# Kernel tuning notes

Measured on AMD Instinct MI355X. Metric: run time of the kernel, lower is better.

## Reference

```python
import jax, jax.numpy as jnp
import numpy as np

KERNEL_SIZE = 13
SIGMA_MIN, SIGMA_MAX = 0.4, 10.0
BETA, THRESHOLD = 0.95, 1.0


@jax.custom_vjp
def spike(x):
    # Heaviside forward, snntorch ATan surrogate backward (alpha=2)
    return (x > 0).astype(x.dtype)

def _spike_fwd(x):
    return spike(x), x

def _spike_bwd(x, g):
    return (g / (1.0 + (jnp.pi * x) ** 2),)

spike.defvjp(_spike_fwd, _spike_bwd)


def setup_inputs() -> dict:
    key = jax.random.key(0)
    k1, k2 = jax.random.split(key)
    B, C, T = 32, 224, 2048
    inp = jax.random.normal(k1, (B, 1, C, T), dtype=jnp.float32)
    linear_w = jax.random.normal(k2, (1, C), dtype=jnp.float32) * (1.0 / np.sqrt(C))
    return {"inp": inp, "linear_w": linear_w}


def _forward(inp, linear_w):
    x = inp[:, 0]  # [B, C, T]
    B, C, T = x.shape
    sigma_mean = 0.5 * (SIGMA_MIN + SIGMA_MAX)
    # adaptive sigma per (batch, time): Linear over channel axis, no bias
    w = sigma_mean + jnp.einsum('bct,c->bt', x, linear_w[0]) * (SIGMA_MAX - SIGMA_MIN)
    w = jnp.clip(w, SIGMA_MIN, SIGMA_MAX)  # [B, T]

    half = KERNEL_SIZE // 2
    r = jnp.linspace(-half, half, KERNEL_SIZE)
    r_all = jnp.linspace(-half * 10, half * 10, KERNEL_SIZE * 10)
    sig = w[..., None]  # [B, T, 1]
    kern = jnp.exp(-0.5 * (r / sig) ** 2)                       # [B, T, K]
    norm = jnp.exp(-0.5 * (r_all / sig) ** 2).sum(-1, keepdims=True)
    kern = kern / norm                                          # normalized over fine grid

    # adaptive gaussian smoothing along the CHANNEL axis (per timestep kernel)
    xt = jnp.transpose(x, (0, 2, 1))                            # [B, T, C]
    padded = jnp.pad(xt, ((0, 0), (0, 0), (half, half)))        # zero pad channels
    x_mean = sum(padded[:, :, k:k + C] * kern[:, :, k:k + 1]
                 for k in range(KERNEL_SIZE))                   # [B, T, C]
    x_mean = jnp.transpose(x_mean, (0, 2, 1))                   # [B, C, T]

    I = x - jax.nn.relu(x - x_mean)                             # soft min(x, x_mean)

    # Leaky-integrate-and-fire over time (snntorch Leaky, reset-by-subtract)
    def step(mem, I_t):
        reset = jax.lax.stop_gradient((mem > THRESHOLD).astype(I_t.dtype))
        mem = BETA * mem + I_t - reset * THRESHOLD
        spk = spike(mem - THRESHOLD)
        return mem, spk

    I_seq = jnp.transpose(I, (2, 0, 1))                         # [T, B, C]
    _, spk = jax.lax.scan(step, jnp.zeros((B, C), I.dtype), I_seq)
    spk = jnp.transpose(spk, (1, 2, 0))                         # [B, C, T]
    return spk[:, None]                                         # [B, 1, C, T]


def reference(inp, linear_w):
    return _forward(inp, linear_w)
```

## Files before the change

kernel.cpp:

```cpp
#include <hip/hip_runtime.h>
#include <math.h>

#define BB 32
#define CCH 224
#define TTT 2048
#define BT (BB*TTT)
#define TPB 64
#define NT  (TTT/TPB)
#define CG  28
#define NCG (CCH/CG)
#define IROW 29
#define RD 4

__global__ __launch_bounds__(256) void kw(
    const float* __restrict__ x, const float* __restrict__ lw,
    double* __restrict__ kernG)
{
    __shared__ double sd[16][64];
    __shared__ float  lws[CCH];
    const int b   = blockIdx.y;
    const int t0  = blockIdx.x * 64;
    const int tid = threadIdx.x;

    if (tid < CCH) lws[tid] = lw[tid];
    __syncthreads();

    {
        const int q = tid & 15, g = tid >> 4;
        const float* xb = x + (((size_t)(b * CCH + g * 14)) << 11) + t0 + 4 * q;
        double a0 = 0, a1 = 0, a2 = 0, a3 = 0;
        #pragma unroll
        for (int i = 0; i < 14; ++i) {
            float4 v = *(const float4*)(xb + ((size_t)i << 11));
            double wv = (double)lws[g * 14 + i];
            a0 += (double)v.x * wv;
            a1 += (double)v.y * wv;
            a2 += (double)v.z * wv;
            a3 += (double)v.w * wv;
        }
        sd[g][4 * q + 0] = a0; sd[g][4 * q + 1] = a1;
        sd[g][4 * q + 2] = a2; sd[g][4 * q + 3] = a3;
    }
    __syncthreads();

    if (tid < 64) {
        const int t = tid;
        double s2 = 0.0;
        #pragma unroll
        for (int g = 0; g < 16; ++g) s2 += sd[g][t];

        double w = 5.2 + s2 * 9.6;
        w = fmin(fmax(w, 0.4), 10.0);
        double iw2 = 1.0 / (w * w);

        const double s = 120.0 / 129.0;
        double G  = exp(-0.125 * s * s * iw2);
        double G2 = G * G, G4 = G2 * G2, G8 = G4 * G4;
        double term = G, cmul = G8, norm = G;
        for (int u = 1; u <= 64; ++u) { term *= cmul; cmul *= G8; norm += term; }
        norm *= 2.0;

        double P = exp(-0.5 * iw2), P2 = P * P;
        double a = 1.0, bm = P, inv = 1.0 / norm;
        double* kr = kernG + (size_t)b * TTT + t0 + t;
        kr[0] = inv;
        #pragma unroll
        for (int d = 1; d <= 6; ++d) {
            a *= bm; bm *= P2;
            kr[(size_t)d * BT] = a * inv;
        }
    }
}

#define PF(h,s) ((h)*RD+(s))
#define CF(s)   (8+(s))
#define SF(s)   (12+(s))
#define OW(s)   (16+(s))

__global__ __launch_bounds__(256) void kf(
    const float* __restrict__ x, const double* __restrict__ kernG,
    float* __restrict__ out)
{
    __shared__ double Is[RD][TPB][IROW];
    __shared__ unsigned long long bitsb[RD][CG];
    __shared__ int fl[32];

    const int b    = blockIdx.y;
    const int c0   = blockIdx.x * CG;
    const int tid  = threadIdx.x;
    const int wid  = tid >> 6;
    const int lane = tid & 63;

    if (tid < 32) fl[tid] = 0;
    __syncthreads();

    const float*  xbase = x + (((size_t)(b * CCH)) << 11);
    const double* kbase = kernG + (size_t)b * TTT;
    float* obase = out + (((size_t)(b * CCH + c0)) << 11);

    if (wid == 1 || wid == 2) {
        const int h  = wid - 1;
        const int cb = 14 * h;
        const int crow0 = c0 + cb - 6;
        float  xc[26], xn[26];
        double kc[7],  kn[7];

        #pragma unroll
        for (int i = 0; i < 26; ++i) {
            int cr = crow0 + i;
            xc[i] = (cr >= 0 && cr < CCH) ? xbase[((size_t)cr << 11) + lane] : 0.0f;
        }
        #pragma unroll
        for (int d = 0; d < 7; ++d) kc[d] = kbase[(size_t)d * BT + lane];

        #pragma unroll 1
        for (int k = 0; k < NT; ++k) {
            if (k + 1 < NT) {
                const int gt = (k + 1) * TPB + lane;
                #pragma unroll
                for (int i = 0; i < 26; ++i) {
                    int cr = crow0 + i;
                    xn[i] = (cr >= 0 && cr < CCH) ? xbase[((size_t)cr << 11) + gt] : 0.0f;
                }
                #pragma unroll
                for (int d = 0; d < 7; ++d) kn[d] = kbase[(size_t)d * BT + gt];
            }
            double iv[14];
            #pragma unroll
            for (int c = 0; c < 14; ++c) {
                double acc = 0.0;
                #pragma unroll
                for (int kk = 0; kk < 13; ++kk) {
                    int d = kk < 6 ? 6 - kk : kk - 6;
                    acc = fma((double)xc[c + kk], kc[d], acc);
                }
                double xvv = (double)xc[c + 6];
                double dd  = xvv - acc;
                iv[c] = xvv - (dd > 0.0 ? dd : 0.0);
            }
            const int s = k & (RD - 1);
            while (__hip_atomic_load(&fl[CF(s)], __ATOMIC_ACQUIRE,
                                     __HIP_MEMORY_SCOPE_WORKGROUP) < k + 1 - RD)
                __builtin_amdgcn_s_sleep(1);
            #pragma unroll
            for (int c = 0; c < 14; ++c) Is[s][lane][cb + c] = iv[c];
            if (lane == 0)
                __hip_atomic_store(&fl[PF(h, s)], k + 1, __ATOMIC_RELEASE,
                                   __HIP_MEMORY_SCOPE_WORKGROUP);
            if (k + 1 < NT) {
                #pragma unroll
                for (int i = 0; i < 26; ++i) xc[i] = xn[i];
                #pragma unroll
                for (int d = 0; d < 7; ++d) kc[d] = kn[d];
            }
        }
    } else if (wid == 0) {
        const int c    = lane;
        const int cidx = (c < CG) ? c : 0;
        double mem = 0.0;
        bool   r   = false;

        #pragma unroll 1
        for (int k = 0; k < NT; ++k) {
            const int s = k & (RD - 1);
            while (__hip_atomic_load(&fl[PF(0, s)], __ATOMIC_ACQUIRE,
                                     __HIP_MEMORY_SCOPE_WORKGROUP) < k + 1 ||
                   __hip_atomic_load(&fl[PF(1, s)], __ATOMIC_ACQUIRE,
                                     __HIP_MEMORY_SCOPE_WORKGROUP) < k + 1)
                __builtin_amdgcn_s_sleep(1);

            unsigned long long bits = 0ull;
            {
                double va[8], vam[8], vb[8], vbm[8];
                #pragma unroll
                for (int j = 0; j < 8; ++j) {
                    va[j] = Is[s][j][cidx]; vam[j] = va[j] - 1.0;
                }
                #pragma unroll
                for (int g = 0; g < 64; g += 16) {
                    #pragma unroll
                    for (int j = 0; j < 8; ++j) {
                        vb[j] = Is[s][g + 8 + j][cidx]; vbm[j] = vb[j] - 1.0;
                    }
                    #pragma unroll
                    for (int j = 0; j < 8; ++j) {
                        double m1 = fma(0.95, mem, va[j]);
                        double m2 = fma(0.95, mem, vam[j]);
                        mem = r ? m2 : m1;
                        r = mem > 1.0;
                        bits |= (unsigned long long)(r ? 1 : 0) << (g + j);
                    }
                    if (g + 16 < 64) {
                        #pragma unroll
                        for (int j = 0; j < 8; ++j) {
                            va[j] = Is[s][g + 16 + j][cidx]; vam[j] = va[j] - 1.0;
                        }
                    }
                    #pragma unroll
                    for (int j = 0; j < 8; ++j) {
                        double m1 = fma(0.95, mem, vb[j]);
                        double m2 = fma(0.95, mem, vbm[j]);
                        mem = r ? m2 : m1;
                        r = mem > 1.0;
                        bits |= (unsigned long long)(r ? 1 : 0) << (g + 8 + j);
                    }
                }
            }
            if (lane == 0)
                __hip_atomic_store(&fl[CF(s)], k + 1, __ATOMIC_RELEASE,
                                   __HIP_MEMORY_SCOPE_WORKGROUP);

            while (__hip_atomic_load(&fl[OW(s)], __ATOMIC_ACQUIRE,
                                     __HIP_MEMORY_SCOPE_WORKGROUP) < k + 1 - RD)
                __builtin_amdgcn_s_sleep(1);
            if (c < CG) bitsb[s][c] = bits;
            if (lane == 0)
                __hip_atomic_store(&fl[SF(s)], k + 1, __ATOMIC_RELEASE,
                                   __HIP_MEMORY_SCOPE_WORKGROUP);
        }
    } else {
        const int qq = lane & 15;
        #pragma unroll 1
        for (int k = 0; k < NT; ++k) {
            const int s = k & (RD - 1);
            while (__hip_atomic_load(&fl[SF(s)], __ATOMIC_ACQUIRE,
                                     __HIP_MEMORY_SCOPE_WORKGROUP) < k + 1)
                __builtin_amdgcn_s_sleep(1);
            unsigned long long bb[7];
            #pragma unroll
            for (int i = 0; i < 7; ++i) {
                int cc = (lane >> 4) + 4 * i;
                bb[i] = bitsb[s][cc];
            }
            if (lane == 0)
                __hip_atomic_store(&fl[OW(s)], k + 1, __ATOMIC_RELEASE,
                                   __HIP_MEMORY_SCOPE_WORKGROUP);
            #pragma unroll
            for (int i = 0; i < 7; ++i) {
                int cc = (lane >> 4) + 4 * i;
                unsigned long long bv = bb[i] >> (4 * qq);
                float4 v;
                v.x = (bv & 1ull) ? 1.0f : 0.0f;
                v.y = (bv & 2ull) ? 1.0f : 0.0f;
                v.z = (bv & 4ull) ? 1.0f : 0.0f;
                v.w = (bv & 8ull) ? 1.0f : 0.0f;
                *(float4*)(obase + ((size_t)cc << 11) + k * TPB + 4 * qq) = v;
            }
        }
    }
}

extern "C" void kernel_launch(void* const* d_in, const int* in_sizes, int n_in,
                              void* d_out, int out_size, void* d_ws, size_t ws_size,
                              hipStream_t stream)
{
    const float* x  = (const float*)d_in[0];
    const float* lw = (const float*)d_in[1];
    float* out = (float*)d_out;

    double* kernG = (double*)d_ws;

    kw<<<dim3(TTT / 64, BB), 256, 0, stream>>>(x, lw, kernG);
    kf<<<dim3(NCG, BB), 256, 0, stream>>>(x, kernG, out);
}
```

Baseline: 157.5 us.

## Use volatile LDS spin flags, ping-pong conv buffers, and retile sigma kernel

Replaces the workgroup-scope atomic acquire/release flag polling and s_sleep in the warp-specialized pipeline with volatile LDS spins plus explicit lgkmcnt waits and compiler fences. The goal is lower handoff latency between the conv warps, the LIF scan warp and the store warp. The conv loop is unrolled by two with A/B register buffers, which removes the per-iteration prefetch register copies. The sigma/kernel-weight kernel now covers 256 timesteps per block with all 256 threads computing the normalisation, using fewer blocks and less idle work. Busy spinning without sleep can steal issue slots from co-resident waves, and the hand-written fences carry memory-ordering risk.

```diff
diff --git a/kernel.cpp b/kernel.cpp
--- a/kernel.cpp
+++ b/kernel.cpp
@@ -12,46 +12,51 @@
 #define IROW 29
 #define RD 4
 
+#define PF(h,s) ((h)*RD+(s))
+#define CF(s)   (8+(s))
+#define SF(s)   (12+(s))
+#define OW(s)   (16+(s))
+
+#define LDS_REL() asm volatile("s_waitcnt lgkmcnt(0)" ::: "memory")
+#define CFENCE()  asm volatile("" ::: "memory")
+
 __global__ __launch_bounds__(256) void kw(
     const float* __restrict__ x, const float* __restrict__ lw,
     double* __restrict__ kernG)
 {
-    __shared__ double sd[16][64];
+    __shared__ double sd[4][256];
     __shared__ float  lws[CCH];
-    const int b   = blockIdx.y;
-    const int t0  = blockIdx.x * 64;
-    const int tid = threadIdx.x;
+    const int b    = blockIdx.y;
+    const int t0   = blockIdx.x << 8;
+    const int tid  = threadIdx.x;
+    const int w    = tid >> 6, lane = tid & 63;
 
     if (tid < CCH) lws[tid] = lw[tid];
     __syncthreads();
 
     {
-        const int q = tid & 15, g = tid >> 4;
-        const float* xb = x + (((size_t)(b * CCH + g * 14)) << 11) + t0 + 4 * q;
+        const float* xb = x + (((size_t)(b * CCH + w)) << 11) + t0 + 4 * lane;
         double a0 = 0, a1 = 0, a2 = 0, a3 = 0;
-        #pragma unroll
-        for (int i = 0; i < 14; ++i) {
-            float4 v = *(const float4*)(xb + ((size_t)i << 11));
-            double wv = (double)lws[g * 14 + i];
+        #pragma unroll 8
+        for (int i = 0; i < 56; ++i) {
+            float4 v = *(const float4*)(xb + ((size_t)(4 * i) << 11));
+            double wv = (double)lws[w + 4 * i];
             a0 += (double)v.x * wv;
             a1 += (double)v.y * wv;
             a2 += (double)v.z * wv;
             a3 += (double)v.w * wv;
         }
-        sd[g][4 * q + 0] = a0; sd[g][4 * q + 1] = a1;
-        sd[g][4 * q + 2] = a2; sd[g][4 * q + 3] = a3;
+        sd[w][4 * lane + 0] = a0; sd[w][4 * lane + 1] = a1;
+        sd[w][4 * lane + 2] = a2; sd[w][4 * lane + 3] = a3;
     }
     __syncthreads();
 
-    if (tid < 64) {
-        const int t = tid;
-        double s2 = 0.0;
-        #pragma unroll
-        for (int g = 0; g < 16; ++g) s2 += sd[g][t];
-
-        double w = 5.2 + s2 * 9.6;
-        w = fmin(fmax(w, 0.4), 10.0);
-        double iw2 = 1.0 / (w * w);
+    {
+        double s2 = (sd[0][tid] + sd[1][tid]) + (sd[2][tid] + sd[3][tid]);
+
+        double w2 = 5.2 + s2 * 9.6;
+        w2 = fmin(fmax(w2, 0.4), 10.0);
+        double iw2 = 1.0 / (w2 * w2);
 
         const double s = 120.0 / 129.0;
         double G  = exp(-0.125 * s * s * iw2);
@@ -62,7 +67,7 @@
 
         double P = exp(-0.5 * iw2), P2 = P * P;
         double a = 1.0, bm = P, inv = 1.0 / norm;
-        double* kr = kernG + (size_t)b * TTT + t0 + t;
+        double* kr = kernG + (size_t)b * TTT + t0 + tid;
         kr[0] = inv;
         #pragma unroll
         for (int d = 1; d <= 6; ++d) {
@@ -72,10 +77,41 @@
     }
 }
 
-#define PF(h,s) ((h)*RD+(s))
-#define CF(s)   (8+(s))
-#define SF(s)   (12+(s))
-#define OW(s)   (16+(s))
+#define CONV_BODY(K, XC, KC, XN, KN)                                       \
+    {                                                                      \
+        const int k_ = (K);                                                \
+        if (k_ + 1 < NT) {                                                 \
+            const int gt = (k_ + 1) * TPB + lane;                          \
+            _Pragma("unroll")                                              \
+            for (int i = 0; i < 26; ++i) {                                 \
+                int cr = crow0 + i;                                        \
+                XN[i] = (cr >= 0 && cr < CCH)                              \
+                    ? xbase[((size_t)cr << 11) + gt] : 0.0f;               \
+            }                                                              \
+            _Pragma("unroll")                                              \
+            for (int d = 0; d < 7; ++d)                                    \
+                KN[d] = kbase[(size_t)d * BT + gt];                        \
+        }                                                                  \
+        double iv[14];                                                     \
+        _Pragma("unroll")                                                  \
+        for (int c = 0; c < 14; ++c) {                                     \
+            double acc = 0.0;                                              \
+            _Pragma("unroll")                                              \
+            for (int kk = 0; kk < 13; ++kk) {                              \
+                int d = kk < 6 ? 6 - kk : kk - 6;                          \
+                acc = fma((double)XC[c + kk], KC[d], acc);                 \
+            }                                                              \
+            double xvv = (double)XC[c + 6];                                \
+            double dd  = xvv - acc;                                        \
+            iv[c] = xvv - (dd > 0.0 ? dd : 0.0);                           \
+        }                                                                  \
+        const int s_ = k_ & (RD - 1);                                      \
+        while (vfl[CF(s_)] < k_ + 1 - RD) {}                               \
+        CFENCE();                                                          \
+        _Pragma("unroll")                                                  \
+        for (int c = 0; c < 14; ++c) Is[s_][lane][cb + c] = iv[c];         \
+        if (lane == 0) { LDS_REL(); vfl[PF(h, s_)] = k_ + 1; }             \
+    }
 
 __global__ __launch_bounds__(256) void kf(
     const float* __restrict__ x, const double* __restrict__ kernG,
@@ -84,6 +120,7 @@
     __shared__ double Is[RD][TPB][IROW];
     __shared__ unsigned long long bitsb[RD][CG];
     __shared__ int fl[32];
+    volatile int* vfl = fl;
 
     const int b    = blockIdx.y;
     const int c0   = blockIdx.x * CG;
@@ -102,57 +139,21 @@
         const int h  = wid - 1;
         const int cb = 14 * h;
         const int crow0 = c0 + cb - 6;
-        float  xc[26], xn[26];
-        double kc[7],  kn[7];
+        float  xcA[26], xcB[26];
+        double kcA[7],  kcB[7];
 
         #pragma unroll
         for (int i = 0; i < 26; ++i) {
             int cr = crow0 + i;
-            xc[i] = (cr >= 0 && cr < CCH) ? xbase[((size_t)cr << 11) + lane] : 0.0f;
+            xcA[i] = (cr >= 0 && cr < CCH) ? xbase[((size_t)cr << 11) + lane] : 0.0f;
         }
         #pragma unroll
-        for (int d = 0; d < 7; ++d) kc[d] = kbase[(size_t)d * BT + lane];
+        for (int d = 0; d < 7; ++d) kcA[d] = kbase[(size_t)d * BT + lane];
 
         #pragma unroll 1
-        for (int k = 0; k < NT; ++k) {
-            if (k + 1 < NT) {
-                const int gt = (k + 1) * TPB + lane;
-                #pragma unroll
-                for (int i = 0; i < 26; ++i) {
-                    int cr = crow0 + i;
-                    xn[i] = (cr >= 0 && cr < CCH) ? xbase[((size_t)cr << 11) + gt] : 0.0f;
-                }
-                #pragma unroll
-                for (int d = 0; d < 7; ++d) kn[d] = kbase[(size_t)d * BT + gt];
-            }
-            double iv[14];
-            #pragma unroll
-            for (int c = 0; c < 14; ++c) {
-                double acc = 0.0;
-                #pragma unroll
-                for (int kk = 0; kk < 13; ++kk) {
-                    int d = kk < 6 ? 6 - kk : kk - 6;
-                    acc = fma((double)xc[c + kk], kc[d], acc);
-                }
-                double xvv = (double)xc[c + 6];
-                double dd  = xvv - acc;
-                iv[c] = xvv - (dd > 0.0 ? dd : 0.0);
-            }
-            const int s = k & (RD - 1);
-            while (__hip_atomic_load(&fl[CF(s)], __ATOMIC_ACQUIRE,
-                                     __HIP_MEMORY_SCOPE_WORKGROUP) < k + 1 - RD)
-                __builtin_amdgcn_s_sleep(1);
-            #pragma unroll
-            for (int c = 0; c < 14; ++c) Is[s][lane][cb + c] = iv[c];
-            if (lane == 0)
-                __hip_atomic_store(&fl[PF(h, s)], k + 1, __ATOMIC_RELEASE,
-                                   __HIP_MEMORY_SCOPE_WORKGROUP);
-            if (k + 1 < NT) {
-                #pragma unroll
-                for (int i = 0; i < 26; ++i) xc[i] = xn[i];
-                #pragma unroll
-                for (int d = 0; d < 7; ++d) kc[d] = kn[d];
-            }
+        for (int k = 0; k < NT; k += 2) {
+            CONV_BODY(k,     xcA, kcA, xcB, kcB)
+            CONV_BODY(k + 1, xcB, kcB, xcA, kcA)
         }
     } else if (wid == 0) {
         const int c    = lane;
@@ -163,11 +164,8 @@
         #pragma unroll 1
         for (int k = 0; k < NT; ++k) {
             const int s = k & (RD - 1);
-            while (__hip_atomic_load(&fl[PF(0, s)], __ATOMIC_ACQUIRE,
-                                     __HIP_MEMORY_SCOPE_WORKGROUP) < k + 1 ||
-                   __hip_atomic_load(&fl[PF(1, s)], __ATOMIC_ACQUIRE,
-                                     __HIP_MEMORY_SCOPE_WORKGROUP) < k + 1)
-                __builtin_amdgcn_s_sleep(1);
+            while (vfl[PF(0, s)] < k + 1 || vfl[PF(1, s)] < k + 1) {}
+            CFENCE();
 
             unsigned long long bits = 0ull;
             {
@@ -206,35 +204,27 @@
                     }
                 }
             }
-            if (lane == 0)
-                __hip_atomic_store(&fl[CF(s)], k + 1, __ATOMIC_RELEASE,
-                                   __HIP_MEMORY_SCOPE_WORKGROUP);
-
-            while (__hip_atomic_load(&fl[OW(s)], __ATOMIC_ACQUIRE,
-                                     __HIP_MEMORY_SCOPE_WORKGROUP) < k + 1 - RD)
-                __builtin_amdgcn_s_sleep(1);
+            if (lane == 0) { LDS_REL(); vfl[CF(s)] = k + 1; }
+
+            while (vfl[OW(s)] < k + 1 - RD) {}
+            CFENCE();
             if (c < CG) bitsb[s][c] = bits;
-            if (lane == 0)
-                __hip_atomic_store(&fl[SF(s)], k + 1, __ATOMIC_RELEASE,
-                                   __HIP_MEMORY_SCOPE_WORKGROUP);
+            if (lane == 0) { LDS_REL(); vfl[SF(s)] = k + 1; }
         }
     } else {
         const int qq = lane & 15;
         #pragma unroll 1
         for (int k = 0; k < NT; ++k) {
             const int s = k & (RD - 1);
-            while (__hip_atomic_load(&fl[SF(s)], __ATOMIC_ACQUIRE,
-                                     __HIP_MEMORY_SCOPE_WORKGROUP) < k + 1)
-                __builtin_amdgcn_s_sleep(1);
+            while (vfl[SF(s)] < k + 1) {}
+            CFENCE();
             unsigned long long bb[7];
             #pragma unroll
             for (int i = 0; i < 7; ++i) {
                 int cc = (lane >> 4) + 4 * i;
                 bb[i] = bitsb[s][cc];
             }
-            if (lane == 0)
-                __hip_atomic_store(&fl[OW(s)], k + 1, __ATOMIC_RELEASE,
-                                   __HIP_MEMORY_SCOPE_WORKGROUP);
+            if (lane == 0) { LDS_REL(); vfl[OW(s)] = k + 1; }
             #pragma unroll
             for (int i = 0; i < 7; ++i) {
                 int cc = (lane >> 4) + 4 * i;
@@ -260,6 +250,6 @@
 
     double* kernG = (double*)d_ws;
 
-    kw<<<dim3(TTT / 64, BB), 256, 0, stream>>>(x, lw, kernG);
+    kw<<<dim3(8, BB), 256, 0, stream>>>(x, lw, kernG);
     kf<<<dim3(NCG, BB), 256, 0, stream>>>(x, kernG, out);
 }
```

Measured after the change: 244.3 us. 1.55x slower.
